# Kernel optimization log

Hardware: AMD Instinct MI355X
Metric: run time of the kernel (lower is better)

The kernel has to match this reference:

```python
import jax, jax.numpy as jnp
import numpy as np
import math

NUM_HEADS = 16
D_MODEL = 1024
BATCH = 1
SEQ_LEN = 4096


def alibi_slopes(num_heads):
    # slopes m_h = (256 ** (1/H)) ** -(h+1)
    x = (2.0 ** 8) ** (1.0 / num_heads)
    return jnp.asarray([1.0 / x ** (i + 1) for i in range(num_heads)], dtype=jnp.float32)


def setup_inputs() -> dict:
    key = jax.random.key(0)
    k1, k2 = jax.random.split(key)
    x = jax.random.normal(k1, (BATCH, SEQ_LEN, D_MODEL), dtype=jnp.float32)
    # nn.Linear(d_model, 3*d_model, bias=False); store as [d_model, 3*d_model] so y = x @ w
    w_kqv = jax.random.normal(k2, (D_MODEL, 3 * D_MODEL), dtype=jnp.float32) * (1.0 / math.sqrt(D_MODEL))
    return {"x": x, "w_kqv": w_kqv}


def reference(x, w_kqv):
    B, S, D = x.shape
    H = NUM_HEADS
    dh = D // H
    scale = jnp.asarray(math.sqrt(D), dtype=x.dtype)  # module divides by sqrt(d_model)

    kqv = x @ w_kqv  # [B, S, 3D]
    # NOTE: original chunks as (key, query, value) in that order
    k, q, v = jnp.split(kqv, 3, axis=-1)
    q = q.reshape(B, S, H, dh)
    k = k.reshape(B, S, H, dh)
    v = v.reshape(B, S, H, dh)

    # ALiBi bias: m_h * (j - i), shape [H, S, S]
    pos = jnp.arange(S)
    rel = pos[None, :] - pos[:, None]  # [S, S], x - y
    slopes = alibi_slopes(H).astype(x.dtype)  # [H]
    bias = slopes[:, None, None] * rel.astype(x.dtype)  # [H, S, S]

    score = jnp.einsum('bihd,bjhd->bhij', q, k) / scale + bias[None]  # [B, H, S, S]
    causal = rel <= 0  # j <= i (lower triangular)
    score = jnp.where(causal[None, None], score, jnp.asarray(-jnp.inf, dtype=score.dtype))

    attn = jax.nn.softmax(score, axis=-1)
    out = jnp.einsum('bhij,bjhd->bihd', attn, v).reshape(B, S, D)
    return out
```

## Files before the change

### kernel.cpp

```cpp
#include <hip/hip_runtime.h>
#include <stdint.h>
#include <math.h>

#define SEQ 4096
#define DM  1024
#define NH  16
#define DH  64
#define LOG2E 1.44269504088896341f

typedef short bf16x8 __attribute__((ext_vector_type(8)));
typedef short bf16x4 __attribute__((ext_vector_type(4)));
typedef float f32x4  __attribute__((ext_vector_type(4)));
typedef uint32_t u32x4 __attribute__((ext_vector_type(4)));

typedef const __attribute__((address_space(1))) short* gptr_t;
typedef __attribute__((address_space(3))) short* lptr_t;

__device__ __forceinline__ short f2bf(float f) {
    union { float f; uint32_t u; } x; x.f = f;
    uint32_t r = (x.u + 0x7fffu + ((x.u >> 16) & 1u)) >> 16;
    return (short)r;
}
__device__ __forceinline__ uint32_t pkbf(float lo, float hi) {
    union { float f; uint32_t u; } a, b; a.f = lo; b.f = hi;
    return (a.u >> 16) | (b.u & 0xffff0000u);
}

__device__ __forceinline__ void load_lds16(const short* g, const short* l) {
    __builtin_amdgcn_global_load_lds((gptr_t)(uintptr_t)g,
                                     (lptr_t)(uint32_t)(uintptr_t)l, 16, 0, 0);
}

__global__ __launch_bounds__(256) void cvt_fused(const float* __restrict__ x,
                                                 const float* __restrict__ w,
                                                 short* __restrict__ xb,
                                                 short* __restrict__ wtb) {
    __shared__ float T[64][69];
    const int b = blockIdx.x;
    if (b < 2048) {
        const int i = (b * 256 + threadIdx.x) * 8;
        float4 a0 = ((const float4*)(x + i))[0];
        float4 a1 = ((const float4*)(x + i))[1];
        bf16x8 p;
        p[0]=f2bf(a0.x); p[1]=f2bf(a0.y); p[2]=f2bf(a0.z); p[3]=f2bf(a0.w);
        p[4]=f2bf(a1.x); p[5]=f2bf(a1.y); p[6]=f2bf(a1.z); p[7]=f2bf(a1.w);
        *(bf16x8*)(xb + i) = p;
        return;
    }
    const int bb = b - 2048;
    const int n0 = (bb % 48) * 64, k0 = (bb / 48) * 64;
    const int t = threadIdx.x;
    {
        const int kr = t >> 4, nc = (t & 15) * 4;
        #pragma unroll
        for (int i = 0; i < 4; ++i) {
            float4 v = *(const float4*)(w + (size_t)(k0 + kr + i * 16) * 3072 + n0 + nc);
            T[kr + i * 16][nc + 0] = v.x; T[kr + i * 16][nc + 1] = v.y;
            T[kr + i * 16][nc + 2] = v.z; T[kr + i * 16][nc + 3] = v.w;
        }
    }
    __syncthreads();
    const int nr = t >> 4, kc = (t & 15) * 4;
    #pragma unroll
    for (int i = 0; i < 4; ++i) {
        const int n = n0 + nr + i * 16;
        const float sc = (n >= 1024 && n < 2048) ? (LOG2E / 32.0f) : 1.0f;
        short4 o;
        o.x = f2bf(T[kc + 0][nr + i * 16] * sc);
        o.y = f2bf(T[kc + 1][nr + i * 16] * sc);
        o.z = f2bf(T[kc + 2][nr + i * 16] * sc);
        o.w = f2bf(T[kc + 3][nr + i * 16] * sc);
        *(short4*)(wtb + (size_t)n * 1024 + k0 + kc) = o;
    }
}

__global__ __launch_bounds__(256) void qkv_gemm(const short* __restrict__ xb,
                                                const short* __restrict__ wtb,
                                                short* __restrict__ kq,
                                                short* __restrict__ vt) {
    __shared__ short As[128 * 64];
    __shared__ short Bs[128 * 64];
    const int col0 = blockIdx.y * 128, row0 = blockIdx.x * 128;
    const int tid = threadIdx.x, w = tid >> 6, lane = tid & 63;
    const int lmod = lane & 15, ldiv = lane >> 4;
    const int wr = (w >> 1) * 64, wc = (w & 1) * 64;

    f32x4 acc[4][4] = {};
    const short* Ag = xb  + (size_t)row0 * DM;
    const short* Bg = wtb + (size_t)col0 * DM;

    for (int k0 = 0; k0 < DM; k0 += 64) {
        __syncthreads();
        #pragma unroll
        for (int t = 0; t < 4; ++t) {
            const int o = (w * 4 + t) * 1024 + lane * 16;
            const int r = o >> 7, cs = (o & 127) >> 1;
            load_lds16(Ag + (size_t)r * DM + k0 + cs, As + (w * 4 + t) * 512);
            load_lds16(Bg + (size_t)r * DM + k0 + cs, Bs + (w * 4 + t) * 512);
        }
        __syncthreads();
        #pragma unroll
        for (int ks = 0; ks < 2; ++ks) {
            bf16x8 af[4], bf[4];
            #pragma unroll
            for (int i = 0; i < 4; ++i)
                af[i] = *(const bf16x8*)(As + (wr + i * 16 + lmod) * 64 + ks * 32 + ldiv * 8);
            #pragma unroll
            for (int j = 0; j < 4; ++j)
                bf[j] = *(const bf16x8*)(Bs + (wc + j * 16 + lmod) * 64 + ks * 32 + ldiv * 8);
            #pragma unroll
            for (int i = 0; i < 4; ++i)
                #pragma unroll
                for (int j = 0; j < 4; ++j)
                    acc[i][j] = __builtin_amdgcn_mfma_f32_16x16x32_bf16(af[i], bf[j], acc[i][j], 0, 0, 0);
        }
    }

    if (col0 < 2048) {
        #pragma unroll
        for (int i = 0; i < 4; ++i)
            #pragma unroll
            for (int j = 0; j < 4; ++j)
                #pragma unroll
                for (int r = 0; r < 4; ++r)
                    kq[(size_t)(row0 + wr + i * 16 + ldiv * 4 + r) * 2048
                       + col0 + wc + j * 16 + lmod] = f2bf(acc[i][j][r]);
    } else {
        #pragma unroll
        for (int i = 0; i < 4; ++i) {
            const int ig = row0 + wr + i * 16 + ldiv * 4;
            #pragma unroll
            for (int j = 0; j < 4; ++j) {
                const int cg = col0 + wc + j * 16 + lmod - 2048;
                const int h = cg >> 6, d = cg & 63;
                bf16x4 p;
                p[0]=f2bf(acc[i][j][0]); p[1]=f2bf(acc[i][j][1]);
                p[2]=f2bf(acc[i][j][2]); p[3]=f2bf(acc[i][j][3]);
                *(bf16x4*)(vt + (size_t)(h * 64 + d) * SEQ + ig) = p;
            }
        }
    }
}

__global__ __launch_bounds__(256, 4) void attn(const short* __restrict__ kq,
                                               const short* __restrict__ vt,
                                               float* __restrict__ o0,
                                               float* __restrict__ o1,
                                               float* __restrict__ ls0,
                                               float* __restrict__ ls1) {
    __shared__ short Ks[64 * 64];
    __shared__ short Vs[64 * 64];

    const int b = blockIdx.x;
    const int band = b >> 8, pos = b & 255, g = pos >> 5;
    const int qt = (band & 1) ? (24 - band * 8 + g) : (31 - band * 8 - g);
    const int h = (pos >> 1) & 15, s = pos & 1;

    const int tid = threadIdx.x, w = tid >> 6, lane = tid & 63;
    const int lmod = lane & 15, ldiv = lane >> 4;
    const float slope2 = exp2f(-0.5f * (float)(h + 1)) * LOG2E;

    const int sr0 = w * 16 + (lane >> 3), sr1 = sr0 + 8;
    const int sc0 = (lane & 7) ^ (sr0 & 7), sc1 = (lane & 7) ^ (sr1 & 7);

    const int xorm = lmod & 7;
    const int cxs0 = (ldiv ^ xorm) * 8;
    const int cxs1 = ((4 + ldiv) ^ xorm) * 8;
    const int vsub = (ldiv & 1) * 4;
    const int vlo[2] = { (((ldiv >> 1)    ) ^ xorm) * 8 + vsub,
                         ((4 + (ldiv >> 1)) ^ xorm) * 8 + vsub };
    const int vhi[2] = { ((2 + (ldiv >> 1)) ^ xorm) * 8 + vsub,
                         ((6 + (ldiv >> 1)) ^ xorm) * 8 + vsub };

    const int rowbase = qt * 128 + w * 32;

    bf16x8 qf[2][2];
    #pragma unroll
    for (int m = 0; m < 2; ++m) {
        const short* qp = kq + (size_t)(rowbase + m * 16 + lmod) * 2048 + 1024 + h * 64;
        qf[m][0] = *(const bf16x8*)(qp + ldiv * 8);
        qf[m][1] = *(const bf16x8*)(qp + 32 + ldiv * 8);
    }
    int db2[2];
    float pre[2][4];
    #pragma unroll
    for (int m = 0; m < 2; ++m) {
        db2[m] = 4 * ldiv - (rowbase + m * 16 + lmod);
        #pragma unroll
        for (int r = 0; r < 4; ++r) pre[m][r] = slope2 * (float)(db2[m] + r);
    }

    f32x4 O[2][4] = {};
    float lsum[2] = {};
    const int kt0 = s ? (qt + 1) : 0;
    const int kt1 = s ? (2 * qt + 2) : (qt + 1);

    for (int kt = kt0; kt < kt1; ++kt) {
        __syncthreads();
        {
            const short* kb = kq + (size_t)(kt * 64) * 2048 + h * 64;
            load_lds16(kb + (size_t)sr0 * 2048 + sc0 * 8, Ks + (w * 16) * 64);
            load_lds16(kb + (size_t)sr1 * 2048 + sc1 * 8, Ks + (w * 16 + 8) * 64);
            const short* vb = vt + (size_t)(h * 64) * SEQ + kt * 64;
            load_lds16(vb + (size_t)sr0 * SEQ + sc0 * 8, Vs + (w * 16) * 64);
            load_lds16(vb + (size_t)sr1 * SEQ + sc1 * 8, Vs + (w * 16 + 8) * 64);
        }
        __syncthreads();

        const bool diag = (kt >= 2 * qt);
        const int dt = kt * 64;
        const float cb = slope2 * (float)dt;

        #pragma unroll
        for (int ks = 0; ks < 2; ++ks) {
            u32x4 pk0, pk1;
            #pragma unroll
            for (int j1 = 0; j1 < 2; ++j1) {
                const int nt = ks * 2 + j1;
                const float cn = cb + slope2 * (float)(nt * 16);
                f32x4 s0, s1;
                #pragma unroll
                for (int r = 0; r < 4; ++r) { s0[r] = pre[0][r] + cn; s1[r] = pre[1][r] + cn; }
                const short* krow = Ks + (nt * 16 + lmod) * 64;
                const bf16x8 kf0 = *(const bf16x8*)(krow + cxs0);
                const bf16x8 kf1 = *(const bf16x8*)(krow + cxs1);
                s0 = __builtin_amdgcn_mfma_f32_16x16x32_bf16(kf0, qf[0][0], s0, 0, 0, 0);
                s0 = __builtin_amdgcn_mfma_f32_16x16x32_bf16(kf1, qf[0][1], s0, 0, 0, 0);
                s1 = __builtin_amdgcn_mfma_f32_16x16x32_bf16(kf0, qf[1][0], s1, 0, 0, 0);
                s1 = __builtin_amdgcn_mfma_f32_16x16x32_bf16(kf1, qf[1][1], s1, 0, 0, 0);

                float p0[4], p1[4];
                if (diag) {
                    #pragma unroll
                    for (int r = 0; r < 4; ++r) {
                        float v0 = s0[r], v1 = s1[r];
                        if (dt + nt * 16 + r + db2[0] > 0) v0 = -1e30f;
                        if (dt + nt * 16 + r + db2[1] > 0) v1 = -1e30f;
                        p0[r] = __builtin_amdgcn_exp2f(v0);
                        p1[r] = __builtin_amdgcn_exp2f(v1);
                    }
                } else {
                    #pragma unroll
                    for (int r = 0; r < 4; ++r) {
                        p0[r] = __builtin_amdgcn_exp2f(s0[r]);
                        p1[r] = __builtin_amdgcn_exp2f(s1[r]);
                    }
                }
                lsum[0] += (p0[0] + p0[1]) + (p0[2] + p0[3]);
                lsum[1] += (p1[0] + p1[1]) + (p1[2] + p1[3]);
                pk0[j1 * 2]     = pkbf(p0[0], p0[1]);
                pk0[j1 * 2 + 1] = pkbf(p0[2], p0[3]);
                pk1[j1 * 2]     = pkbf(p1[0], p1[1]);
                pk1[j1 * 2 + 1] = pkbf(p1[2], p1[3]);
            }
            const bf16x8 pa0 = __builtin_bit_cast(bf16x8, pk0);
            const bf16x8 pa1 = __builtin_bit_cast(bf16x8, pk1);
            #pragma unroll
            for (int nt2 = 0; nt2 < 4; ++nt2) {
                const short* vrow = Vs + (nt2 * 16 + lmod) * 64;
                const bf16x4 lo = *(const bf16x4*)(vrow + vlo[ks]);
                const bf16x4 hi = *(const bf16x4*)(vrow + vhi[ks]);
                const bf16x8 vf = __builtin_shufflevector(lo, hi, 0, 1, 2, 3, 4, 5, 6, 7);
                O[0][nt2] = __builtin_amdgcn_mfma_f32_16x16x32_bf16(pa0, vf, O[0][nt2], 0, 0, 0);
                O[1][nt2] = __builtin_amdgcn_mfma_f32_16x16x32_bf16(pa1, vf, O[1][nt2], 0, 0, 0);
            }
        }
    }

    #pragma unroll
    for (int m = 0; m < 2; ++m) {
        float v = lsum[m];
        v += __shfl_xor(v, 16);
        v += __shfl_xor(v, 32);
        lsum[m] = v;
    }

    float* ob = s ? o1 : o0;
    float* lb = s ? ls1 : ls0;
    #pragma unroll
    for (int m = 0; m < 2; ++m) {
        const int i0 = rowbase + m * 16 + ldiv * 4;
        #pragma unroll
        for (int nt2 = 0; nt2 < 4; ++nt2)
            #pragma unroll
            for (int r = 0; r < 4; ++r)
                ob[(size_t)(i0 + r) * DM + h * 64 + nt2 * 16 + lmod] = O[m][nt2][r];
    }
    if (ldiv == 0) {
        #pragma unroll
        for (int m = 0; m < 2; ++m)
            lb[h * SEQ + rowbase + m * 16 + lmod] = lsum[m];
    }
}

__global__ __launch_bounds__(256) void combine(float* __restrict__ out,
                                               const float* __restrict__ opart,
                                               const float* __restrict__ ls0,
                                               const float* __restrict__ ls1) {
    const int i8 = (blockIdx.x * 256 + threadIdx.x) * 8;
    const int row = i8 >> 10, col = i8 & 1023, h = col >> 6;
    const float l = ls0[h * SEQ + row] + ls1[h * SEQ + row];
    const float rc = 1.0f / l;
    float4 a0 = *(const float4*)(out + i8);
    float4 a1 = *(const float4*)(out + i8 + 4);
    float4 b0 = *(const float4*)(opart + i8);
    float4 b1 = *(const float4*)(opart + i8 + 4);
    float4 c0, c1;
    c0.x = (a0.x + b0.x) * rc; c0.y = (a0.y + b0.y) * rc;
    c0.z = (a0.z + b0.z) * rc; c0.w = (a0.w + b0.w) * rc;
    c1.x = (a1.x + b1.x) * rc; c1.y = (a1.y + b1.y) * rc;
    c1.z = (a1.z + b1.z) * rc; c1.w = (a1.w + b1.w) * rc;
    *(float4*)(out + i8) = c0;
    *(float4*)(out + i8 + 4) = c1;
}

extern "C" void kernel_launch(void* const* d_in, const int* in_sizes, int n_in,
                              void* d_out, int out_size, void* d_ws, size_t ws_size,
                              hipStream_t stream) {
    const float* x = (const float*)d_in[0];
    const float* w = (const float*)d_in[1];
    float* out = (float*)d_out;

    char* ws = (char*)d_ws;
    short* kq    = (short*)(ws);
    short* vt    = (short*)(ws + ((size_t)16 << 20));
    short* xb    = (short*)(ws + ((size_t)24 << 20));
    short* wtb   = (short*)(ws + ((size_t)32 << 20));
    float* opart = (float*)(ws + ((size_t)24 << 20));
    float* ls0   = (float*)(ws + ((size_t)40 << 20));
    float* ls1   = (float*)(ws + ((size_t)40 << 20) + (256 << 10));

    cvt_fused<<<2048 + 768, 256, 0, stream>>>(x, w, xb, wtb);
    qkv_gemm <<<dim3(SEQ / 128, 3072 / 128), 256, 0, stream>>>(xb, wtb, kq, vt);
    attn     <<<1024, 256, 0, stream>>>(kq, vt, out, opart, ls0, ls1);
    combine  <<<SEQ * DM / (256 * 8), 256, 0, stream>>>(out, opart, ls0, ls1);
}
```

Before: 194.8 us.

## Double-buffer K/V tiles in attention and permute V layout for single-load fragments

The attention kernel now double-buffers the K and V LDS tiles, prefetching the next tile while computing the current one, and uses one barrier per iteration instead of two. The GEMM epilogue writes V^T with a permuted key order so each lane reads its P@V fragment as one 16-byte LDS load instead of two 8-byte loads plus a shuffle. P is packed to bf16 with the hardware v_cvt_pk_bf16_f32 instruction, which rounds, where the old code truncated. Row sums are kept as vector accumulators and s_setprio is raised around the MFMA section. Doubling the LDS buffers (32 KB per block) may reduce occupancy at 4 blocks per CU.

```diff
diff --git a/kernel.cpp b/kernel.cpp
--- a/kernel.cpp
+++ b/kernel.cpp
@@ -21,9 +21,10 @@
     uint32_t r = (x.u + 0x7fffu + ((x.u >> 16) & 1u)) >> 16;
     return (short)r;
 }
-__device__ __forceinline__ uint32_t pkbf(float lo, float hi) {
-    union { float f; uint32_t u; } a, b; a.f = lo; b.f = hi;
-    return (a.u >> 16) | (b.u & 0xffff0000u);
+__device__ __forceinline__ uint32_t cvtpk(float lo, float hi) {
+    uint32_t r;
+    asm("v_cvt_pk_bf16_f32 %0, %1, %2" : "=v"(r) : "v"(lo), "v"(hi));
+    return r;
 }
 
 __device__ __forceinline__ void load_lds16(const short* g, const short* l) {
@@ -129,6 +130,9 @@
         #pragma unroll
         for (int i = 0; i < 4; ++i) {
             const int ig = row0 + wr + i * 16 + ldiv * 4;
+            const int kk = ig & 63;
+            const int kkp = (kk & 32) | ((kk & 12) << 1) | ((kk & 16) >> 2);
+            const int igp = (ig & ~63) | kkp;
             #pragma unroll
             for (int j = 0; j < 4; ++j) {
                 const int cg = col0 + wc + j * 16 + lmod - 2048;
@@ -136,7 +140,7 @@
                 bf16x4 p;
                 p[0]=f2bf(acc[i][j][0]); p[1]=f2bf(acc[i][j][1]);
                 p[2]=f2bf(acc[i][j][2]); p[3]=f2bf(acc[i][j][3]);
-                *(bf16x4*)(vt + (size_t)(h * 64 + d) * SEQ + ig) = p;
+                *(bf16x4*)(vt + (size_t)(h * 64 + d) * SEQ + igp) = p;
             }
         }
     }
@@ -148,8 +152,8 @@
                                                float* __restrict__ o1,
                                                float* __restrict__ ls0,
                                                float* __restrict__ ls1) {
-    __shared__ short Ks[64 * 64];
-    __shared__ short Vs[64 * 64];
+    __shared__ short Ks[2][64 * 64];
+    __shared__ short Vs[2][64 * 64];
 
     const int b = blockIdx.x;
     const int band = b >> 8, pos = b & 255, g = pos >> 5;
@@ -166,11 +170,6 @@
     const int xorm = lmod & 7;
     const int cxs0 = (ldiv ^ xorm) * 8;
     const int cxs1 = ((4 + ldiv) ^ xorm) * 8;
-    const int vsub = (ldiv & 1) * 4;
-    const int vlo[2] = { (((ldiv >> 1)    ) ^ xorm) * 8 + vsub,
-                         ((4 + (ldiv >> 1)) ^ xorm) * 8 + vsub };
-    const int vhi[2] = { ((2 + (ldiv >> 1)) ^ xorm) * 8 + vsub,
-                         ((6 + (ldiv >> 1)) ^ xorm) * 8 + vsub };
 
     const int rowbase = qt * 128 + w * 32;
 
@@ -182,35 +181,42 @@
         qf[m][1] = *(const bf16x8*)(qp + 32 + ldiv * 8);
     }
     int db2[2];
-    float pre[2][4];
+    f32x4 pre4[2];
     #pragma unroll
     for (int m = 0; m < 2; ++m) {
         db2[m] = 4 * ldiv - (rowbase + m * 16 + lmod);
         #pragma unroll
-        for (int r = 0; r < 4; ++r) pre[m][r] = slope2 * (float)(db2[m] + r);
+        for (int r = 0; r < 4; ++r) pre4[m][r] = slope2 * (float)(db2[m] + r);
     }
 
     f32x4 O[2][4] = {};
-    float lsum[2] = {};
+    f32x4 ls4[2] = {};
     const int kt0 = s ? (qt + 1) : 0;
     const int kt1 = s ? (2 * qt + 2) : (qt + 1);
 
+    auto stage = [&](int kt_, int p) {
+        const short* kb = kq + (size_t)(kt_ * 64) * 2048 + h * 64;
+        load_lds16(kb + (size_t)sr0 * 2048 + sc0 * 8, &Ks[p][(w * 16) * 64]);
+        load_lds16(kb + (size_t)sr1 * 2048 + sc1 * 8, &Ks[p][(w * 16 + 8) * 64]);
+        const short* vb = vt + (size_t)(h * 64) * SEQ + kt_ * 64;
+        load_lds16(vb + (size_t)sr0 * SEQ + sc0 * 8, &Vs[p][(w * 16) * 64]);
+        load_lds16(vb + (size_t)sr1 * SEQ + sc1 * 8, &Vs[p][(w * 16 + 8) * 64]);
+    };
+
+    stage(kt0, 0);
+    __syncthreads();
+    int par = 0;
+
     for (int kt = kt0; kt < kt1; ++kt) {
-        __syncthreads();
-        {
-            const short* kb = kq + (size_t)(kt * 64) * 2048 + h * 64;
-            load_lds16(kb + (size_t)sr0 * 2048 + sc0 * 8, Ks + (w * 16) * 64);
-            load_lds16(kb + (size_t)sr1 * 2048 + sc1 * 8, Ks + (w * 16 + 8) * 64);
-            const short* vb = vt + (size_t)(h * 64) * SEQ + kt * 64;
-            load_lds16(vb + (size_t)sr0 * SEQ + sc0 * 8, Vs + (w * 16) * 64);
-            load_lds16(vb + (size_t)sr1 * SEQ + sc1 * 8, Vs + (w * 16 + 8) * 64);
-        }
-        __syncthreads();
+        const short* Kb = &Ks[par][0];
+        const short* Vb = &Vs[par][0];
+        if (kt + 1 < kt1) stage(kt + 1, par ^ 1);
 
         const bool diag = (kt >= 2 * qt);
         const int dt = kt * 64;
         const float cb = slope2 * (float)dt;
 
+        __builtin_amdgcn_s_setprio(1);
         #pragma unroll
         for (int ks = 0; ks < 2; ++ks) {
             u32x4 pk0, pk1;
@@ -218,10 +224,9 @@
             for (int j1 = 0; j1 < 2; ++j1) {
                 const int nt = ks * 2 + j1;
                 const float cn = cb + slope2 * (float)(nt * 16);
-                f32x4 s0, s1;
-                #pragma unroll
-                for (int r = 0; r < 4; ++r) { s0[r] = pre[0][r] + cn; s1[r] = pre[1][r] + cn; }
-                const short* krow = Ks + (nt * 16 + lmod) * 64;
+                f32x4 s0 = pre4[0] + cn;
+                f32x4 s1 = pre4[1] + cn;
+                const short* krow = Kb + (nt * 16 + lmod) * 64;
                 const bf16x8 kf0 = *(const bf16x8*)(krow + cxs0);
                 const bf16x8 kf1 = *(const bf16x8*)(krow + cxs1);
                 s0 = __builtin_amdgcn_mfma_f32_16x16x32_bf16(kf0, qf[0][0], s0, 0, 0, 0);
@@ -229,7 +234,7 @@
                 s1 = __builtin_amdgcn_mfma_f32_16x16x32_bf16(kf0, qf[1][0], s1, 0, 0, 0);
                 s1 = __builtin_amdgcn_mfma_f32_16x16x32_bf16(kf1, qf[1][1], s1, 0, 0, 0);
 
-                float p0[4], p1[4];
+                f32x4 p0, p1;
                 if (diag) {
                     #pragma unroll
                     for (int r = 0; r < 4; ++r) {
@@ -246,30 +251,33 @@
                         p1[r] = __builtin_amdgcn_exp2f(s1[r]);
                     }
                 }
-                lsum[0] += (p0[0] + p0[1]) + (p0[2] + p0[3]);
-                lsum[1] += (p1[0] + p1[1]) + (p1[2] + p1[3]);
-                pk0[j1 * 2]     = pkbf(p0[0], p0[1]);
-                pk0[j1 * 2 + 1] = pkbf(p0[2], p0[3]);
-                pk1[j1 * 2]     = pkbf(p1[0], p1[1]);
-                pk1[j1 * 2 + 1] = pkbf(p1[2], p1[3]);
+                ls4[0] += p0;
+                ls4[1] += p1;
+                pk0[j1 * 2]     = cvtpk(p0[0], p0[1]);
+                pk0[j1 * 2 + 1] = cvtpk(p0[2], p0[3]);
+                pk1[j1 * 2]     = cvtpk(p1[0], p1[1]);
+                pk1[j1 * 2 + 1] = cvtpk(p1[2], p1[3]);
             }
             const bf16x8 pa0 = __builtin_bit_cast(bf16x8, pk0);
             const bf16x8 pa1 = __builtin_bit_cast(bf16x8, pk1);
+            const int cxo = ks ? cxs1 : cxs0;
             #pragma unroll
             for (int nt2 = 0; nt2 < 4; ++nt2) {
-                const short* vrow = Vs + (nt2 * 16 + lmod) * 64;
-                const bf16x4 lo = *(const bf16x4*)(vrow + vlo[ks]);
-                const bf16x4 hi = *(const bf16x4*)(vrow + vhi[ks]);
-                const bf16x8 vf = __builtin_shufflevector(lo, hi, 0, 1, 2, 3, 4, 5, 6, 7);
+                const bf16x8 vf = *(const bf16x8*)(Vb + (nt2 * 16 + lmod) * 64 + cxo);
                 O[0][nt2] = __builtin_amdgcn_mfma_f32_16x16x32_bf16(pa0, vf, O[0][nt2], 0, 0, 0);
                 O[1][nt2] = __builtin_amdgcn_mfma_f32_16x16x32_bf16(pa1, vf, O[1][nt2], 0, 0, 0);
             }
         }
-    }
-
+        __builtin_amdgcn_s_setprio(0);
+
+        __syncthreads();
+        par ^= 1;
+    }
+
+    float lsum[2];
     #pragma unroll
     for (int m = 0; m < 2; ++m) {
-        float v = lsum[m];
+        float v = (ls4[m][0] + ls4[m][1]) + (ls4[m][2] + ls4[m][3]);
         v += __shfl_xor(v, 16);
         v += __shfl_xor(v, 32);
         lsum[m] = v;
```

Result: slower. 212.3 us (+9.0%).
